# Performance work log

Measured on AMD Instinct MI355X. Metric: run time of the kernel, lower is better.

Reference implementation:

```python
import jax, jax.numpy as jnp
import numpy as np

N = 50000      # nodes
E = 800000     # edges (avg degree 16)
D_IN = 128
H = 128
D_OUT = 64
L = 3          # num GCNConv layers


def setup_inputs() -> dict:
    key = jax.random.key(0)
    ks = jax.random.split(key, 9)
    x = jax.random.normal(ks[0], (N, D_IN), jnp.float32)
    edge_index = jax.random.randint(ks[1], (2, E), 0, N, dtype=jnp.int32)
    s_in = 1.0 / np.sqrt(D_IN)
    s_h = 1.0 / np.sqrt(H)
    W1 = jax.random.normal(ks[2], (D_IN, H), jnp.float32) * s_in
    b1 = jnp.zeros((H,), jnp.float32)
    Wc = jax.random.normal(ks[3], (L, H, H), jnp.float32) * s_h
    bc = jnp.zeros((L, H), jnp.float32)
    W2 = jax.random.normal(ks[4], (H, D_OUT), jnp.float32) * s_h
    b2 = jnp.zeros((D_OUT,), jnp.float32)
    return {"x": x, "edge_index": edge_index, "W1": W1, "b1": b1,
            "Wc": Wc, "bc": bc, "W2": W2, "b2": b2}


def reference(x, edge_index, W1, b1, Wc, bc, W2, b2):
    n = x.shape[0]
    src, dst = edge_index[0], edge_index[1]
    # GCNConv normalization with self-loops: deg[i] = 1 + in-degree(i)
    deg = jnp.zeros((n,), x.dtype).at[dst].add(1.0) + 1.0
    dis = jax.lax.rsqrt(deg)                       # D^{-1/2}
    norm = dis[src] * dis[dst]                     # per-edge norm, [E]
    self_norm = (dis * dis)[:, None]               # self-loop norm, [n,1]
    # dnn1: Linear + ReLU
    h = jax.nn.relu(x @ W1 + b1)
    # GCNConv layers: x' = D^{-1/2}(A+I)D^{-1/2} X W + b
    for l in range(Wc.shape[0]):
        hw = h @ Wc[l]                             # [n, H]
        msg = hw[src] * norm[:, None]              # gather + scale, [E, H]
        agg = jax.ops.segment_sum(msg, dst, num_segments=n)
        h = agg + self_norm * hw + bc[l]
    # dnn2: Linear
    return h @ W2 + b2
```

## Files before the change

kernel.cpp:

```cpp
#include <hip/hip_runtime.h>
#include <hip/hip_fp16.h>


typedef _Float16 f16;
typedef __attribute__((ext_vector_type(8))) _Float16 f16x8;
typedef __attribute__((ext_vector_type(4))) float f32x4;

constexpr int H = 128;
constexpr int CH = 512;


__global__ __launch_bounds__(256) void k_degree(const int* __restrict__ dst,
                                                int* __restrict__ cnt, int E) {
    int e = blockIdx.x * 256 + threadIdx.x;
    if (e < E) atomicAdd(&cnt[dst[e]], 1);
}

__global__ __launch_bounds__(256) void k_dis(const int* __restrict__ cnt,
                                             float* __restrict__ dis,
                                             float* __restrict__ dis2, int n) {
    int i = blockIdx.x * 256 + threadIdx.x;
    if (i < n) {
        float d = (float)(cnt[i] + 1);
        float r = rsqrtf(d);
        dis[i] = r;
        dis2[i] = r * r;
    }
}

__global__ __launch_bounds__(CH) void k_scan1(const int* __restrict__ cnt,
                                              int* __restrict__ roff,
                                              int* __restrict__ csum, int n) {
    __shared__ int sh[CH];
    int t = threadIdx.x;
    int i = blockIdx.x * CH + t;
    int v = (i < n) ? cnt[i] : 0;
    sh[t] = v;
    __syncthreads();
    for (int off = 1; off < CH; off <<= 1) {
        int x = (t >= off) ? sh[t - off] : 0;
        __syncthreads();
        sh[t] += x;
        __syncthreads();
    }
    if (i < n) roff[i] = sh[t] - v;
    if (t == CH - 1) csum[blockIdx.x] = sh[t];
}

__global__ __launch_bounds__(256) void k_scan2(const int* __restrict__ csum,
                                               int* __restrict__ coff, int nch) {
    __shared__ int sh[256];
    int t = threadIdx.x;
    int v = (t < nch) ? csum[t] : 0;
    sh[t] = v;
    __syncthreads();
    for (int off = 1; off < 256; off <<= 1) {
        int x = (t >= off) ? sh[t - off] : 0;
        __syncthreads();
        sh[t] += x;
        __syncthreads();
    }
    if (t < nch) coff[t] = sh[t] - v;
}

__global__ __launch_bounds__(256) void k_scan3(int* __restrict__ roff,
                                               const int* __restrict__ coff,
                                               int n, int E) {
    int i = blockIdx.x * 256 + threadIdx.x;
    if (i < n) roff[i] += coff[i / CH];
    if (i == 0) roff[n] = E;
}

__global__ __launch_bounds__(256) void k_fill(const int* __restrict__ src,
                                              const int* __restrict__ dst,
                                              const int* __restrict__ roff,
                                              int* __restrict__ fil,
                                              const float* __restrict__ dis,
                                              int2* __restrict__ edata, int E) {
    int e = blockIdx.x * 256 + threadIdx.x;
    if (e < E) {
        int d = dst[e], s = src[e];
        int pos = roff[d] + atomicAdd(&fil[d], 1);
        float nm = dis[s] * dis[d];
        edata[pos] = make_int2(s, __float_as_int(nm));
    }
}


__global__ __launch_bounds__(256) void k_cvt_x(const float* __restrict__ x,
                                               f16* __restrict__ xh, int total8) {
    int i = blockIdx.x * 256 + threadIdx.x;
    if (i < total8) {
        float4 a = *(const float4*)&x[(size_t)i * 8];
        float4 b = *(const float4*)&x[(size_t)i * 8 + 4];
        f16x8 o;
        o[0] = (f16)a.x; o[1] = (f16)a.y; o[2] = (f16)a.z; o[3] = (f16)a.w;
        o[4] = (f16)b.x; o[5] = (f16)b.y; o[6] = (f16)b.z; o[7] = (f16)b.w;
        *(f16x8*)&xh[(size_t)i * 8] = o;
    }
}

__global__ __launch_bounds__(256) void k_cvt_w(const float* __restrict__ W1,
                                               const float* __restrict__ Wc,
                                               const float* __restrict__ W2,
                                               f16* __restrict__ BT1,
                                               f16* __restrict__ BTc,
                                               f16* __restrict__ BT2) {
    int i = blockIdx.x * 256 + threadIdx.x;
    if (i < 16384) {
        int c = i >> 7, k = i & 127;
        BT1[i] = (f16)W1[k * 128 + c];
    } else if (i < 65536) {
        int j = i - 16384;
        int l = j >> 14, r = j & 16383;
        int c = r >> 7, k = r & 127;
        BTc[j] = (f16)Wc[l * 16384 + k * 128 + c];
    } else if (i < 73728) {
        int j = i - 65536;
        int c = j >> 7, k = j & 127;
        BT2[j] = (f16)W2[k * 64 + c];
    }
}


template <int NCOLS, int MODE>
__global__ __launch_bounds__(256) void k_gemm16(const f16* __restrict__ A,
                                                const f16* __restrict__ BT,
                                                const float* __restrict__ bias,
                                                void* __restrict__ Cv, int n) {
    constexpr int CT = NCOLS / 16;
    constexpr int BSTR = H + 8;
    __shared__ f16 Bs[NCOLS * BSTR];

    const int tid = threadIdx.x;
    constexpr int CHUNKS = NCOLS * H / (256 * 8);
#pragma unroll
    for (int it = 0; it < CHUNKS; ++it) {
        int idx = tid + it * 256;
        int r = idx >> 4;
        int c8 = idx & 15;
        *(f16x8*)&Bs[r * BSTR + c8 * 8] = *(const f16x8*)&BT[r * H + c8 * 8];
    }
    __syncthreads();

    const int l = tid & 63;
    const int w = tid >> 6;
    const int lrow = l & 15;
    const int lk = (l >> 4) * 8;
    int arow = blockIdx.x * 64 + w * 16 + lrow;
    int arc = arow < n ? arow : n - 1;
    const f16* ap = A + (size_t)arc * H;

    f16x8 a[4];
#pragma unroll
    for (int ks = 0; ks < 4; ++ks) a[ks] = *(const f16x8*)&ap[ks * 32 + lk];

    f32x4 acc[CT];
#pragma unroll
    for (int ct = 0; ct < CT; ++ct) acc[ct] = (f32x4)(0.f);

#pragma unroll
    for (int ks = 0; ks < 4; ++ks) {
#pragma unroll
        for (int ct = 0; ct < CT; ++ct) {
            f16x8 b = *(const f16x8*)&Bs[(ct * 16 + lrow) * BSTR + ks * 32 + lk];
            acc[ct] = __builtin_amdgcn_mfma_f32_16x16x32_f16(a[ks], b, acc[ct], 0, 0, 0);
        }
    }

    const int rbase = blockIdx.x * 64 + w * 16 + (l >> 4) * 4;
#pragma unroll
    for (int ct = 0; ct < CT; ++ct) {
        int col = ct * 16 + lrow;
        float bv = 0.f;
        if constexpr (MODE != 0) bv = bias[col];
#pragma unroll
        for (int r = 0; r < 4; ++r) {
            int row = rbase + r;
            if (row >= n) continue;
            float v = acc[ct][r] + bv;
            if constexpr (MODE == 1) v = fmaxf(v, 0.f);
            if constexpr (MODE == 2)
                ((float*)Cv)[(size_t)row * NCOLS + col] = v;
            else
                ((f16*)Cv)[(size_t)row * NCOLS + col] = (f16)v;
        }
    }
}


__global__ __launch_bounds__(256) void k_agg16(const __half2* __restrict__ hw,
                                               const int* __restrict__ roff,
                                               const int2* __restrict__ edata,
                                               const float* __restrict__ dis2,
                                               const float* __restrict__ bias,
                                               __half2* __restrict__ hout, int n) {
    int wave = threadIdx.x >> 6;
    int lane = threadIdx.x & 63;
    int node = blockIdx.x * 4 + wave;
    if (node >= n) return;

    int e0 = roff[node];
    int e1 = roff[node + 1];

    float2 sv = __half22float2(hw[(size_t)node * 64 + lane]);
    float d2 = dis2[node];
    float ax = sv.x * d2, ay = sv.y * d2;

    int e = e0;
    for (; e + 4 <= e1; e += 4) {
        int2 ed0 = edata[e], ed1 = edata[e + 1], ed2 = edata[e + 2], ed3 = edata[e + 3];
        float2 v0 = __half22float2(hw[(size_t)ed0.x * 64 + lane]);
        float2 v1 = __half22float2(hw[(size_t)ed1.x * 64 + lane]);
        float2 v2 = __half22float2(hw[(size_t)ed2.x * 64 + lane]);
        float2 v3 = __half22float2(hw[(size_t)ed3.x * 64 + lane]);
        float n0 = __int_as_float(ed0.y), n1 = __int_as_float(ed1.y);
        float n2 = __int_as_float(ed2.y), n3 = __int_as_float(ed3.y);
        ax = fmaf(n0, v0.x, ax); ay = fmaf(n0, v0.y, ay);
        ax = fmaf(n1, v1.x, ax); ay = fmaf(n1, v1.y, ay);
        ax = fmaf(n2, v2.x, ax); ay = fmaf(n2, v2.y, ay);
        ax = fmaf(n3, v3.x, ax); ay = fmaf(n3, v3.y, ay);
    }
    for (; e < e1; ++e) {
        int2 ed = edata[e];
        float2 v = __half22float2(hw[(size_t)ed.x * 64 + lane]);
        float nm = __int_as_float(ed.y);
        ax = fmaf(nm, v.x, ax); ay = fmaf(nm, v.y, ay);
    }

    float2 b = ((const float2*)bias)[lane];
    ax += b.x; ay += b.y;
    hout[(size_t)node * 64 + lane] = __float22half2_rn(make_float2(ax, ay));
}


extern "C" void kernel_launch(void* const* d_in, const int* in_sizes, int n_in,
                              void* d_out, int out_size, void* d_ws, size_t ws_size,
                              hipStream_t stream) {
    const float* x  = (const float*)d_in[0];
    const int*   ei = (const int*)d_in[1];
    const float* W1 = (const float*)d_in[2];
    const float* b1 = (const float*)d_in[3];
    const float* Wc = (const float*)d_in[4];
    const float* bc = (const float*)d_in[5];
    const float* W2 = (const float*)d_in[6];
    const float* b2 = (const float*)d_in[7];
    float* out = (float*)d_out;

    const int n = in_sizes[0] / H;
    const int E = in_sizes[1] / 2;
    const int* src = ei;
    const int* dst = ei + E;

    char* p = (char*)d_ws;
    auto alloc = [&](size_t b) -> void* {
        void* r = (void*)p;
        p += (b + 255) & ~(size_t)255;
        return r;
    };
    f16*   xh   = (f16*)alloc((size_t)n * H * 2);
    f16*   h    = (f16*)alloc((size_t)n * H * 2);
    f16*   hw   = (f16*)alloc((size_t)n * H * 2);
    f16*   BT1  = (f16*)alloc(16384 * 2);
    f16*   BTc  = (f16*)alloc(3 * 16384 * 2);
    f16*   BT2  = (f16*)alloc(8192 * 2);
    int*   cnt  = (int*)alloc((size_t)n * 4);
    int*   roff = (int*)alloc((size_t)(n + 1) * 4);
    int*   fil  = (int*)alloc((size_t)n * 4);
    const int nch = (n + CH - 1) / CH;
    int*   csum = (int*)alloc((size_t)nch * 4);
    int*   coff = (int*)alloc((size_t)nch * 4);
    int2*  edata = (int2*)alloc((size_t)E * 8);
    float* dis  = (float*)alloc((size_t)n * 4);
    float* dis2 = (float*)alloc((size_t)n * 4);

    hipMemsetAsync(cnt, 0, (size_t)n * 4, stream);
    hipMemsetAsync(fil, 0, (size_t)n * 4, stream);

    k_degree<<<(E + 255) / 256, 256, 0, stream>>>(dst, cnt, E);
    k_dis<<<(n + 255) / 256, 256, 0, stream>>>(cnt, dis, dis2, n);
    k_scan1<<<nch, CH, 0, stream>>>(cnt, roff, csum, n);
    k_scan2<<<1, 256, 0, stream>>>(csum, coff, nch);
    k_scan3<<<(n + 255) / 256, 256, 0, stream>>>(roff, coff, n, E);
    k_fill<<<(E + 255) / 256, 256, 0, stream>>>(src, dst, roff, fil, dis, edata, E);

    k_cvt_x<<<(n * H / 8 + 255) / 256, 256, 0, stream>>>(x, xh, n * H / 8);
    k_cvt_w<<<288, 256, 0, stream>>>(W1, Wc, W2, BT1, BTc, BT2);

    const int gblk = (n + 63) / 64;
    k_gemm16<128, 1><<<gblk, 256, 0, stream>>>(xh, BT1, b1, h, n);
    for (int l = 0; l < 3; ++l) {
        k_gemm16<128, 0><<<gblk, 256, 0, stream>>>(h, BTc + (size_t)l * 16384, nullptr, hw, n);
        k_agg16<<<(n + 3) / 4, 256, 0, stream>>>((const __half2*)hw, roff, edata, dis2,
                                                 bc + (size_t)l * H, (__half2*)h, n);
    }
    k_gemm16<64, 2><<<gblk, 256, 0, stream>>>(h, BT2, b2, out, n);
}
```

Measured before the change: 344.3 us.

## Fuse preprocessing kernels, record atomic ranks, and unroll aggregation with nontemporal loads

Records each edge's slot in k_degree from the atomicAdd return value. This removes the second atomic pass and the fil memset in the CSR fill. It also folds the dis computation into scan1 and folds the fp32-to-fp16 conversion of x into the first GEMM, removing two kernels and an intermediate buffer. The aggregation loop is unrolled to 8 and uses nontemporal loads and stores, while the fill switches to a 64-bit atomicExch store that may cost more than a plain store.

```diff
diff --git a/kernel.cpp b/kernel.cpp
--- a/kernel.cpp
+++ b/kernel.cpp
@@ -11,30 +11,26 @@
 
 
 __global__ __launch_bounds__(256) void k_degree(const int* __restrict__ dst,
-                                                int* __restrict__ cnt, int E) {
+                                                int* __restrict__ cnt,
+                                                int* __restrict__ rank, int E) {
     int e = blockIdx.x * 256 + threadIdx.x;
-    if (e < E) atomicAdd(&cnt[dst[e]], 1);
-}
-
-__global__ __launch_bounds__(256) void k_dis(const int* __restrict__ cnt,
-                                             float* __restrict__ dis,
-                                             float* __restrict__ dis2, int n) {
-    int i = blockIdx.x * 256 + threadIdx.x;
-    if (i < n) {
-        float d = (float)(cnt[i] + 1);
-        float r = rsqrtf(d);
-        dis[i] = r;
-        dis2[i] = r * r;
-    }
+    if (e < E) rank[e] = atomicAdd(&cnt[dst[e]], 1);
 }
 
 __global__ __launch_bounds__(CH) void k_scan1(const int* __restrict__ cnt,
                                               int* __restrict__ roff,
-                                              int* __restrict__ csum, int n) {
+                                              int* __restrict__ csum,
+                                              float* __restrict__ dis,
+                                              float* __restrict__ dis2, int n) {
     __shared__ int sh[CH];
     int t = threadIdx.x;
     int i = blockIdx.x * CH + t;
     int v = (i < n) ? cnt[i] : 0;
+    if (i < n) {
+        float r = rsqrtf((float)(v + 1));
+        dis[i] = r;
+        dis2[i] = r * r;
+    }
     sh[t] = v;
     __syncthreads();
     for (int off = 1; off < CH; off <<= 1) {
@@ -73,32 +69,22 @@
 
 __global__ __launch_bounds__(256) void k_fill(const int* __restrict__ src,
                                               const int* __restrict__ dst,
+                                              const int* __restrict__ rank,
                                               const int* __restrict__ roff,
-                                              int* __restrict__ fil,
                                               const float* __restrict__ dis,
-                                              int2* __restrict__ edata, int E) {
+                                              unsigned long long* __restrict__ edata,
+                                              int E) {
     int e = blockIdx.x * 256 + threadIdx.x;
     if (e < E) {
         int d = dst[e], s = src[e];
-        int pos = roff[d] + atomicAdd(&fil[d], 1);
+        int pos = roff[d] + rank[e];
         float nm = dis[s] * dis[d];
-        edata[pos] = make_int2(s, __float_as_int(nm));
-    }
-}
-
-
-__global__ __launch_bounds__(256) void k_cvt_x(const float* __restrict__ x,
-                                               f16* __restrict__ xh, int total8) {
-    int i = blockIdx.x * 256 + threadIdx.x;
-    if (i < total8) {
-        float4 a = *(const float4*)&x[(size_t)i * 8];
-        float4 b = *(const float4*)&x[(size_t)i * 8 + 4];
-        f16x8 o;
-        o[0] = (f16)a.x; o[1] = (f16)a.y; o[2] = (f16)a.z; o[3] = (f16)a.w;
-        o[4] = (f16)b.x; o[5] = (f16)b.y; o[6] = (f16)b.z; o[7] = (f16)b.w;
-        *(f16x8*)&xh[(size_t)i * 8] = o;
-    }
-}
+        unsigned long long v = (unsigned long long)(unsigned)s |
+                               ((unsigned long long)__float_as_uint(nm) << 32);
+        atomicExch(&edata[pos], v);
+    }
+}
+
 
 __global__ __launch_bounds__(256) void k_cvt_w(const float* __restrict__ W1,
                                                const float* __restrict__ Wc,
@@ -123,8 +109,8 @@
 }
 
 
-template <int NCOLS, int MODE>
-__global__ __launch_bounds__(256) void k_gemm16(const f16* __restrict__ A,
+template <int NCOLS, int MODE, bool AF32>
+__global__ __launch_bounds__(256) void k_gemm16(const void* __restrict__ Av,
                                                 const f16* __restrict__ BT,
                                                 const float* __restrict__ bias,
                                                 void* __restrict__ Cv, int n) {
@@ -149,11 +135,24 @@
     const int lk = (l >> 4) * 8;
     int arow = blockIdx.x * 64 + w * 16 + lrow;
     int arc = arow < n ? arow : n - 1;
-    const f16* ap = A + (size_t)arc * H;
 
     f16x8 a[4];
-#pragma unroll
-    for (int ks = 0; ks < 4; ++ks) a[ks] = *(const f16x8*)&ap[ks * 32 + lk];
+    if constexpr (AF32) {
+        const float* ap = (const float*)Av + (size_t)arc * H;
+#pragma unroll
+        for (int ks = 0; ks < 4; ++ks) {
+            float4 u = *(const float4*)&ap[ks * 32 + lk];
+            float4 v = *(const float4*)&ap[ks * 32 + lk + 4];
+            f16x8 t;
+            t[0] = (f16)u.x; t[1] = (f16)u.y; t[2] = (f16)u.z; t[3] = (f16)u.w;
+            t[4] = (f16)v.x; t[5] = (f16)v.y; t[6] = (f16)v.z; t[7] = (f16)v.w;
+            a[ks] = t;
+        }
+    } else {
+        const f16* ap = (const f16*)Av + (size_t)arc * H;
+#pragma unroll
+        for (int ks = 0; ks < 4; ++ks) a[ks] = *(const f16x8*)&ap[ks * 32 + lk];
+    }
 
     f32x4 acc[CT];
 #pragma unroll
@@ -191,10 +190,10 @@
 
 __global__ __launch_bounds__(256) void k_agg16(const __half2* __restrict__ hw,
                                                const int* __restrict__ roff,
-                                               const int2* __restrict__ edata,
+                                               const long long* __restrict__ edata,
                                                const float* __restrict__ dis2,
                                                const float* __restrict__ bias,
-                                               __half2* __restrict__ hout, int n) {
+                                               unsigned int* __restrict__ hout, int n) {
     int wave = threadIdx.x >> 6;
     int lane = threadIdx.x & 63;
     int node = blockIdx.x * 4 + wave;
@@ -208,29 +207,43 @@
     float ax = sv.x * d2, ay = sv.y * d2;
 
     int e = e0;
-    for (; e + 4 <= e1; e += 4) {
-        int2 ed0 = edata[e], ed1 = edata[e + 1], ed2 = edata[e + 2], ed3 = edata[e + 3];
-        float2 v0 = __half22float2(hw[(size_t)ed0.x * 64 + lane]);
-        float2 v1 = __half22float2(hw[(size_t)ed1.x * 64 + lane]);
-        float2 v2 = __half22float2(hw[(size_t)ed2.x * 64 + lane]);
-        float2 v3 = __half22float2(hw[(size_t)ed3.x * 64 + lane]);
-        float n0 = __int_as_float(ed0.y), n1 = __int_as_float(ed1.y);
-        float n2 = __int_as_float(ed2.y), n3 = __int_as_float(ed3.y);
-        ax = fmaf(n0, v0.x, ax); ay = fmaf(n0, v0.y, ay);
-        ax = fmaf(n1, v1.x, ax); ay = fmaf(n1, v1.y, ay);
-        ax = fmaf(n2, v2.x, ax); ay = fmaf(n2, v2.y, ay);
-        ax = fmaf(n3, v3.x, ax); ay = fmaf(n3, v3.y, ay);
+    for (; e + 8 <= e1; e += 8) {
+        long long ed[8];
+#pragma unroll
+        for (int j = 0; j < 8; ++j) ed[j] = __builtin_nontemporal_load(&edata[e + j]);
+        float2 v[8];
+#pragma unroll
+        for (int j = 0; j < 8; ++j)
+            v[j] = __half22float2(hw[(size_t)(unsigned)(ed[j] & 0xffffffff) * 64 + lane]);
+#pragma unroll
+        for (int j = 0; j < 8; ++j) {
+            float nm = __int_as_float((int)(ed[j] >> 32));
+            ax = fmaf(nm, v[j].x, ax);
+            ay = fmaf(nm, v[j].y, ay);
+        }
+    }
+    for (; e + 2 <= e1; e += 2) {
+        long long d0 = __builtin_nontemporal_load(&edata[e]);
+        long long d1 = __builtin_nontemporal_load(&edata[e + 1]);
+        float2 v0 = __half22float2(hw[(size_t)(unsigned)(d0 & 0xffffffff) * 64 + lane]);
+        float2 v1 = __half22float2(hw[(size_t)(unsigned)(d1 & 0xffffffff) * 64 + lane]);
+        ax = fmaf(__int_as_float((int)(d0 >> 32)), v0.x, ax);
+        ay = fmaf(__int_as_float((int)(d0 >> 32)), v0.y, ay);
+        ax = fmaf(__int_as_float((int)(d1 >> 32)), v1.x, ax);
+        ay = fmaf(__int_as_float((int)(d1 >> 32)), v1.y, ay);
     }
     for (; e < e1; ++e) {
-        int2 ed = edata[e];
-        float2 v = __half22float2(hw[(size_t)ed.x * 64 + lane]);
-        float nm = __int_as_float(ed.y);
-        ax = fmaf(nm, v.x, ax); ay = fmaf(nm, v.y, ay);
+        long long d0 = __builtin_nontemporal_load(&edata[e]);
+        float2 v0 = __half22float2(hw[(size_t)(unsigned)(d0 & 0xffffffff) * 64 + lane]);
+        float nm = __int_as_float((int)(d0 >> 32));
+        ax = fmaf(nm, v0.x, ax);
+        ay = fmaf(nm, v0.y, ay);
     }
 
     float2 b = ((const float2*)bias)[lane];
     ax += b.x; ay += b.y;
-    hout[(size_t)node * 64 + lane] = __float22half2_rn(make_float2(ax, ay));
+    __half2 r = __float22half2_rn(make_float2(ax, ay));
+    __builtin_nontemporal_store(*(unsigned int*)&r, &hout[(size_t)node * 64 + lane]);
 }
 
 
@@ -258,41 +271,37 @@
         p += (b + 255) & ~(size_t)255;
         return r;
     };
-    f16*   xh   = (f16*)alloc((size_t)n * H * 2);
     f16*   h    = (f16*)alloc((size_t)n * H * 2);
     f16*   hw   = (f16*)alloc((size_t)n * H * 2);
     f16*   BT1  = (f16*)alloc(16384 * 2);
     f16*   BTc  = (f16*)alloc(3 * 16384 * 2);
     f16*   BT2  = (f16*)alloc(8192 * 2);
     int*   cnt  = (int*)alloc((size_t)n * 4);
+    int*   rank = (int*)alloc((size_t)E * 4);
     int*   roff = (int*)alloc((size_t)(n + 1) * 4);
-    int*   fil  = (int*)alloc((size_t)n * 4);
     const int nch = (n + CH - 1) / CH;
     int*   csum = (int*)alloc((size_t)nch * 4);
     int*   coff = (int*)alloc((size_t)nch * 4);
-    int2*  edata = (int2*)alloc((size_t)E * 8);
+    unsigned long long* edata = (unsigned long long*)alloc((size_t)E * 8);
     float* dis  = (float*)alloc((size_t)n * 4);
     float* dis2 = (float*)alloc((size_t)n * 4);
 
     hipMemsetAsync(cnt, 0, (size_t)n * 4, stream);
-    hipMemsetAsync(fil, 0, (size_t)n * 4, stream);
-
-    k_degree<<<(E + 255) / 256, 256, 0, stream>>>(dst, cnt, E);
-    k_dis<<<(n + 255) / 256, 256, 0, stream>>>(cnt, dis, dis2, n);
-    k_scan1<<<nch, CH, 0, stream>>>(cnt, roff, csum, n);
+
+    k_degree<<<(E + 255) / 256, 256, 0, stream>>>(dst, cnt, rank, E);
+    k_scan1<<<nch, CH, 0, stream>>>(cnt, roff, csum, dis, dis2, n);
     k_scan2<<<1, 256, 0, stream>>>(csum, coff, nch);
     k_scan3<<<(n + 255) / 256, 256, 0, stream>>>(roff, coff, n, E);
-    k_fill<<<(E + 255) / 256, 256, 0, stream>>>(src, dst, roff, fil, dis, edata, E);
-
-    k_cvt_x<<<(n * H / 8 + 255) / 256, 256, 0, stream>>>(x, xh, n * H / 8);
+    k_fill<<<(E + 255) / 256, 256, 0, stream>>>(src, dst, rank, roff, dis, edata, E);
+
     k_cvt_w<<<288, 256, 0, stream>>>(W1, Wc, W2, BT1, BTc, BT2);
 
     const int gblk = (n + 63) / 64;
-    k_gemm16<128, 1><<<gblk, 256, 0, stream>>>(xh, BT1, b1, h, n);
+    k_gemm16<128, 1, true><<<gblk, 256, 0, stream>>>(x, BT1, b1, h, n);
     for (int l = 0; l < 3; ++l) {
-        k_gemm16<128, 0><<<gblk, 256, 0, stream>>>(h, BTc + (size_t)l * 16384, nullptr, hw, n);
-        k_agg16<<<(n + 3) / 4, 256, 0, stream>>>((const __half2*)hw, roff, edata, dis2,
-                                                 bc + (size_t)l * H, (__half2*)h, n);
-    }
-    k_gemm16<64, 2><<<gblk, 256, 0, stream>>>(h, BT2, b2, out, n);
-}
+        k_gemm16<128, 0, false><<<gblk, 256, 0, stream>>>(h, BTc + (size_t)l * 16384, nullptr, hw, n);
+        k_agg16<<<(n + 3) / 4, 256, 0, stream>>>((const __half2*)hw, roff, (const long long*)edata,
+                                                 dis2, bc + (size_t)l * H, (unsigned int*)h, n);
+    }
+    k_gemm16<64, 2, false><<<gblk, 256, 0, stream>>>(h, BT2, b2, out, n);
+}
```

Measured after the change: 337.6 us. Within noise of the previous version (-2.0%).
